# Kernel optimization log

Hardware: AMD Instinct MI355X
Metric: run time of the kernel (lower is better)

The kernel has to match this reference:

```python
import jax, jax.numpy as jnp
import numpy as np

B, C, H, W = 32, 256, 64, 64
K = 7  # kernel_size

def setup_inputs() -> dict:
    key = jax.random.key(0)
    kx, kw = jax.random.split(key)
    x = jax.random.normal(kx, (B, C, H, W), dtype=jnp.float32)
    # Conv2d(2, 1, 7, bias=False) weight: [out_ch=1, in_ch=2, 7, 7]
    w = jax.random.normal(kw, (1, 2, K, K), dtype=jnp.float32) * (1.0 / np.sqrt(2 * K * K))
    return {"x": x, "w": w}

def reference(x, w):
    # channel-wise max and mean, keepdim -> [B,1,H,W]
    max_out = jnp.max(x, axis=1, keepdims=True)
    avg_out = jnp.mean(x, axis=1, keepdims=True)
    concat = jnp.concatenate([max_out, avg_out], axis=1)  # [B,2,H,W]
    pad = K // 2
    conv = jax.lax.conv_general_dilated(
        concat, w,
        window_strides=(1, 1),
        padding=[(pad, pad), (pad, pad)],
        dimension_numbers=("NCHW", "OIHW", "NCHW"),
    )  # [B,1,H,W]
    scale = jax.nn.sigmoid(conv)
    return x * scale  # broadcast over channels
```

## Files before the change

kernel.cpp:

```cpp
#include <hip/hip_runtime.h>
#include <math.h>

constexpr int Bn  = 32;
constexpr int Cn  = 256;
constexpr int Hn  = 64;
constexpr int Wn  = 64;
constexpr int HW  = Hn * Wn;
constexpr int CHW = Cn * HW;
constexpr int HW4 = HW / 4;
constexpr int NPOS  = Bn * HW;
constexpr int NPOS4 = NPOS / 4;

__global__ __launch_bounds__(256) void reduce_k(const float* __restrict__ x,
                                                float* __restrict__ pmax,
                                                float* __restrict__ pavg) {
    __shared__ float4 smax[4][64];
    __shared__ float4 ssum[4][64];

    const int lane  = threadIdx.x & 63;
    const int chunk = threadIdx.x >> 6;
    const int pos4  = blockIdx.x * 64 + lane;
    const int b     = pos4 >> 10;
    const int sp4   = pos4 & (HW4 - 1);

    const float4* xp = (const float4*)x + (size_t)b * (CHW / 4)
                       + (size_t)(chunk * 64) * HW4 + sp4;

    float4 mx = make_float4(-INFINITY, -INFINITY, -INFINITY, -INFINITY);
    float4 sm = make_float4(0.f, 0.f, 0.f, 0.f);

    #pragma unroll 8
    for (int c = 0; c < 64; ++c) {
        float4 v = xp[(size_t)c * HW4];
        mx.x = fmaxf(mx.x, v.x); mx.y = fmaxf(mx.y, v.y);
        mx.z = fmaxf(mx.z, v.z); mx.w = fmaxf(mx.w, v.w);
        sm.x += v.x; sm.y += v.y; sm.z += v.z; sm.w += v.w;
    }

    smax[chunk][lane] = mx;
    ssum[chunk][lane] = sm;
    __syncthreads();

    if (chunk == 0) {
        float4 M = smax[0][lane];
        float4 S = ssum[0][lane];
        #pragma unroll
        for (int k = 1; k < 4; ++k) {
            float4 m2 = smax[k][lane];
            float4 s2 = ssum[k][lane];
            M.x = fmaxf(M.x, m2.x); M.y = fmaxf(M.y, m2.y);
            M.z = fmaxf(M.z, m2.z); M.w = fmaxf(M.w, m2.w);
            S.x += s2.x; S.y += s2.y; S.z += s2.z; S.w += s2.w;
        }
        const float inv = 1.0f / (float)Cn;
        float4 A = make_float4(S.x * inv, S.y * inv, S.z * inv, S.w * inv);
        ((float4*)pmax)[pos4] = M;
        ((float4*)pavg)[pos4] = A;
    }
}

__global__ __launch_bounds__(256) void conv_k(const float* __restrict__ pmax,
                                              const float* __restrict__ pavg,
                                              const float* __restrict__ w,
                                              float* __restrict__ scale) {
    __shared__ float sw[98];
    if (threadIdx.x < 98) sw[threadIdx.x] = w[threadIdx.x];
    __syncthreads();

    const int idx = blockIdx.x * blockDim.x + threadIdx.x;
    const int b   = idx >> 12;
    const int sp  = idx & 4095;
    const int h   = sp >> 6;
    const int wc  = sp & 63;

    const float* pm = pmax + b * HW;
    const float* pa = pavg + b * HW;

    float acc = 0.f;
    #pragma unroll
    for (int kh = 0; kh < 7; ++kh) {
        const int hh = h + kh - 3;
        if (hh < 0 || hh >= Hn) continue;
        #pragma unroll
        for (int kw = 0; kw < 7; ++kw) {
            const int ww = wc + kw - 3;
            if (ww < 0 || ww >= Wn) continue;
            const int o = hh * Wn + ww;
            acc += pm[o] * sw[kh * 7 + kw] + pa[o] * sw[49 + kh * 7 + kw];
        }
    }
    scale[idx] = 1.f / (1.f + expf(-acc));
}

__global__ __launch_bounds__(256) void mul_k(const float* __restrict__ x,
                                             const float* __restrict__ scale,
                                             float* __restrict__ out) {
    const long long i4 = (long long)blockIdx.x * 256 + threadIdx.x;
    const int b   = (int)(i4 >> 18);
    const int hw4 = (int)(i4 & (HW4 - 1));

    const float4 s = ((const float4*)scale)[b * HW4 + hw4];
    const float4 v = ((const float4*)x)[i4];
    float4 o;
    o.x = v.x * s.x; o.y = v.y * s.y; o.z = v.z * s.z; o.w = v.w * s.w;
    ((float4*)out)[i4] = o;
}

extern "C" void kernel_launch(void* const* d_in, const int* in_sizes, int n_in,
                              void* d_out, int out_size, void* d_ws, size_t ws_size,
                              hipStream_t stream) {
    const float* x = (const float*)d_in[0];
    const float* w = (const float*)d_in[1];
    float* out = (float*)d_out;

    float* pmax  = (float*)d_ws;
    float* pavg  = pmax + NPOS;
    float* scale = pavg + NPOS;

    reduce_k<<<NPOS4 / 64, 256, 0, stream>>>(x, pmax, pavg);

    conv_k<<<NPOS / 256, 256, 0, stream>>>(pmax, pavg, w, scale);

    mul_k<<<(Bn * CHW / 4) / 256, 256, 0, stream>>>(x, scale, out);
}
```

Measured before the change: 253.1 us.

## Fuse reduce, conv and multiply into one cooperative kernel with grid syncs

```diff
diff --git a/kernel.cpp b/kernel.cpp
--- a/kernel.cpp
+++ b/kernel.cpp
@@ -1,5 +1,8 @@
 #include <hip/hip_runtime.h>
+#include <hip/hip_cooperative_groups.h>
 #include <math.h>
+
+namespace cg = cooperative_groups;
 
 constexpr int Bn  = 32;
 constexpr int Cn  = 256;
@@ -10,6 +13,119 @@
 constexpr int HW4 = HW / 4;
 constexpr int NPOS  = Bn * HW;
 constexpr int NPOS4 = NPOS / 4;
+
+constexpr int GRID = 512;
+constexpr int BLK  = 256;
+
+__global__ __launch_bounds__(BLK) void fused_k(const float* __restrict__ x,
+                                               const float* __restrict__ w,
+                                               float* __restrict__ out,
+                                               float* __restrict__ pmax,
+                                               float* __restrict__ pavg,
+                                               float* __restrict__ scale) {
+    __shared__ float4 smax[4][64];
+    __shared__ float4 ssum[4][64];
+    __shared__ float  sw[98];
+
+    const int tid = threadIdx.x;
+    if (tid < 98) sw[tid] = w[tid];
+
+    {
+        const int lane  = tid & 63;
+        const int chunk = tid >> 6;
+        const int pos4  = blockIdx.x * 64 + lane;
+        const int b     = pos4 >> 10;
+        const int sp4   = pos4 & (HW4 - 1);
+
+        const float4* xp = (const float4*)x + (size_t)b * (CHW / 4)
+                           + (size_t)(chunk * 64) * HW4 + sp4;
+
+        float4 mx = make_float4(-INFINITY, -INFINITY, -INFINITY, -INFINITY);
+        float4 sm = make_float4(0.f, 0.f, 0.f, 0.f);
+
+        #pragma unroll 8
+        for (int c = 0; c < 64; ++c) {
+            float4 v = xp[(size_t)c * HW4];
+            mx.x = fmaxf(mx.x, v.x); mx.y = fmaxf(mx.y, v.y);
+            mx.z = fmaxf(mx.z, v.z); mx.w = fmaxf(mx.w, v.w);
+            sm.x += v.x; sm.y += v.y; sm.z += v.z; sm.w += v.w;
+        }
+
+        smax[chunk][lane] = mx;
+        ssum[chunk][lane] = sm;
+        __syncthreads();
+
+        if (chunk == 0) {
+            float4 M = smax[0][lane];
+            float4 S = ssum[0][lane];
+            #pragma unroll
+            for (int k = 1; k < 4; ++k) {
+                float4 m2 = smax[k][lane];
+                float4 s2 = ssum[k][lane];
+                M.x = fmaxf(M.x, m2.x); M.y = fmaxf(M.y, m2.y);
+                M.z = fmaxf(M.z, m2.z); M.w = fmaxf(M.w, m2.w);
+                S.x += s2.x; S.y += s2.y; S.z += s2.z; S.w += s2.w;
+            }
+            const float inv = 1.0f / (float)Cn;
+            float4 A = make_float4(S.x * inv, S.y * inv, S.z * inv, S.w * inv);
+            ((float4*)pmax)[pos4] = M;
+            ((float4*)pavg)[pos4] = A;
+        }
+    }
+
+    cg::this_grid().sync();
+
+    {
+        const int idx = blockIdx.x * BLK + tid;
+        const int b   = idx >> 12;
+        const int sp  = idx & 4095;
+        const int h   = sp >> 6;
+        const int wc  = sp & 63;
+
+        const float* pm = pmax + b * HW;
+        const float* pa = pavg + b * HW;
+
+        float acc = 0.f;
+        #pragma unroll
+        for (int kh = 0; kh < 7; ++kh) {
+            const int hh = h + kh - 3;
+            if (hh < 0 || hh >= Hn) continue;
+            #pragma unroll
+            for (int kw = 0; kw < 7; ++kw) {
+                const int ww = wc + kw - 3;
+                if (ww < 0 || ww >= Wn) continue;
+                const int o = hh * Wn + ww;
+                acc += pm[o] * sw[kh * 7 + kw] + pa[o] * sw[49 + kh * 7 + kw];
+            }
+        }
+        scale[idx] = 1.f / (1.f + expf(-acc));
+    }
+
+    cg::this_grid().sync();
+
+    {
+        const int t     = blockIdx.x * BLK + tid;
+        const int hw4   = t & (HW4 - 1);
+        const int cgrp  = t >> 10;
+        const float4* x4 = (const float4*)x;
+        const float4* s4 = (const float4*)scale;
+        float4* o4 = (float4*)out;
+
+        for (int b = 0; b < Bn; ++b) {
+            const float4 s = s4[(b << 10) + hw4];
+            #pragma unroll
+            for (int k = 0; k < 2; ++k) {
+                const size_t i4 = (size_t)b * (CHW / 4)
+                                + (size_t)(cgrp + (k << 7)) * HW4 + hw4;
+                const float4 v = x4[i4];
+                float4 o;
+                o.x = v.x * s.x; o.y = v.y * s.y;
+                o.z = v.z * s.z; o.w = v.w * s.w;
+                o4[i4] = o;
+            }
+        }
+    }
+}
 
 __global__ __launch_bounds__(256) void reduce_k(const float* __restrict__ x,
                                                 float* __restrict__ pmax,
@@ -117,9 +233,15 @@
     float* pavg  = pmax + NPOS;
     float* scale = pavg + NPOS;
 
-    reduce_k<<<NPOS4 / 64, 256, 0, stream>>>(x, pmax, pavg);
-
-    conv_k<<<NPOS / 256, 256, 0, stream>>>(pmax, pavg, w, scale);
-
-    mul_k<<<(Bn * CHW / 4) / 256, 256, 0, stream>>>(x, scale, out);
-}
+    void* args[] = { (void*)&x, (void*)&w, (void*)&out,
+                     (void*)&pmax, (void*)&pavg, (void*)&scale };
+
+    hipError_t err = hipLaunchCooperativeKernel((const void*)fused_k,
+                                                dim3(GRID), dim3(BLK),
+                                                args, 0, stream);
+    if (err != hipSuccess) {
+        reduce_k<<<NPOS4 / 64, 256, 0, stream>>>(x, pmax, pavg);
+        conv_k<<<NPOS / 256, 256, 0, stream>>>(pmax, pavg, w, scale);
+        mul_k<<<(Bn * CHW / 4) / 256, 256, 0, stream>>>(x, scale, out);
+    }
+}
```

New measurement: 385.7 us. +52.4%, slower.

## Fuse conv+sigmoid into the broadcast multiply kernel with shared-memory halo tiles

Applied to the files above, without the earlier changes.

```diff
diff --git a/kernel.cpp b/kernel.cpp
--- a/kernel.cpp
+++ b/kernel.cpp
@@ -10,6 +10,13 @@
 constexpr int HW4 = HW / 4;
 constexpr int NPOS  = Bn * HW;
 constexpr int NPOS4 = NPOS / 4;
+
+constexpr int ROWS   = 16;
+constexpr int NSTR   = Hn / ROWS;
+constexpr int CGRP   = 16;
+constexpr int NCG    = Cn / CGRP;
+constexpr int HALO   = 3;
+constexpr int LROWS  = ROWS + 2 * HALO;
 
 __global__ __launch_bounds__(256) void reduce_k(const float* __restrict__ x,
                                                 float* __restrict__ pmax,
@@ -59,51 +66,74 @@
     }
 }
 
-__global__ __launch_bounds__(256) void conv_k(const float* __restrict__ pmax,
-                                              const float* __restrict__ pavg,
-                                              const float* __restrict__ w,
-                                              float* __restrict__ scale) {
+__global__ __launch_bounds__(256, 8) void convmul_k(const float* __restrict__ x,
+                                                    const float* __restrict__ pmax,
+                                                    const float* __restrict__ pavg,
+                                                    const float* __restrict__ w,
+                                                    float* __restrict__ out) {
+    __shared__ float spm[LROWS * Wn];
+    __shared__ float spa[LROWS * Wn];
+    __shared__ float ssc[ROWS * Wn];
     __shared__ float sw[98];
-    if (threadIdx.x < 98) sw[threadIdx.x] = w[threadIdx.x];
-    __syncthreads();
 
-    const int idx = blockIdx.x * blockDim.x + threadIdx.x;
-    const int b   = idx >> 12;
-    const int sp  = idx & 4095;
-    const int h   = sp >> 6;
-    const int wc  = sp & 63;
+    const int tid = threadIdx.x;
+    const int bid = blockIdx.x;
+    const int cg     = bid & (NCG - 1);
+    const int stripe = (bid >> 4) & (NSTR - 1);
+    const int b      = bid >> 6;
+    const int r0     = stripe * ROWS;
+
+    if (tid < 98) sw[tid] = w[tid];
 
     const float* pm = pmax + b * HW;
     const float* pa = pavg + b * HW;
+    for (int i = tid; i < LROWS * Wn; i += 256) {
+        const int lr  = i >> 6;
+        const int col = i & 63;
+        const int gh  = r0 - HALO + lr;
+        const bool ok = (gh >= 0) && (gh < Hn);
+        spm[i] = ok ? pm[gh * Wn + col] : 0.f;
+        spa[i] = ok ? pa[gh * Wn + col] : 0.f;
+    }
+    __syncthreads();
 
-    float acc = 0.f;
     #pragma unroll
-    for (int kh = 0; kh < 7; ++kh) {
-        const int hh = h + kh - 3;
-        if (hh < 0 || hh >= Hn) continue;
+    for (int p = tid; p < ROWS * Wn; p += 256) {
+        const int hl  = p >> 6;
+        const int col = p & 63;
+        float acc = 0.f;
         #pragma unroll
-        for (int kw = 0; kw < 7; ++kw) {
-            const int ww = wc + kw - 3;
-            if (ww < 0 || ww >= Wn) continue;
-            const int o = hh * Wn + ww;
-            acc += pm[o] * sw[kh * 7 + kw] + pa[o] * sw[49 + kh * 7 + kw];
+        for (int kh = 0; kh < 7; ++kh) {
+            const int lr = hl + kh;
+            #pragma unroll
+            for (int kw = 0; kw < 7; ++kw) {
+                const int ww = col + kw - 3;
+                if (ww < 0 || ww >= Wn) continue;
+                const int o = lr * Wn + ww;
+                acc += spm[o] * sw[kh * 7 + kw] + spa[o] * sw[49 + kh * 7 + kw];
+            }
         }
+        ssc[p] = 1.f / (1.f + expf(-acc));
     }
-    scale[idx] = 1.f / (1.f + expf(-acc));
-}
+    __syncthreads();
 
-__global__ __launch_bounds__(256) void mul_k(const float* __restrict__ x,
-                                             const float* __restrict__ scale,
-                                             float* __restrict__ out) {
-    const long long i4 = (long long)blockIdx.x * 256 + threadIdx.x;
-    const int b   = (int)(i4 >> 18);
-    const int hw4 = (int)(i4 & (HW4 - 1));
+    const float4 s = ((const float4*)ssc)[tid];
 
-    const float4 s = ((const float4*)scale)[b * HW4 + hw4];
-    const float4 v = ((const float4*)x)[i4];
-    float4 o;
-    o.x = v.x * s.x; o.y = v.y * s.y; o.z = v.z * s.z; o.w = v.w * s.w;
-    ((float4*)out)[i4] = o;
+    const size_t base = (size_t)b * (CHW / 4)
+                      + (size_t)(cg * CGRP) * HW4
+                      + (size_t)stripe * (ROWS * Wn / 4) + tid;
+    const float4* x4 = (const float4*)x;
+    float4* o4 = (float4*)out;
+
+    #pragma unroll 4
+    for (int ch = 0; ch < CGRP; ++ch) {
+        const size_t i4 = base + (size_t)ch * HW4;
+        const float4 v = x4[i4];
+        float4 o;
+        o.x = v.x * s.x; o.y = v.y * s.y;
+        o.z = v.z * s.z; o.w = v.w * s.w;
+        o4[i4] = o;
+    }
 }
 
 extern "C" void kernel_launch(void* const* d_in, const int* in_sizes, int n_in,
@@ -113,13 +143,10 @@
     const float* w = (const float*)d_in[1];
     float* out = (float*)d_out;
 
-    float* pmax  = (float*)d_ws;
-    float* pavg  = pmax + NPOS;
-    float* scale = pavg + NPOS;
+    float* pmax = (float*)d_ws;
+    float* pavg = pmax + NPOS;
 
     reduce_k<<<NPOS4 / 64, 256, 0, stream>>>(x, pmax, pavg);
 
-    conv_k<<<NPOS / 256, 256, 0, stream>>>(pmax, pavg, w, scale);
-
-    mul_k<<<(Bn * CHW / 4) / 256, 256, 0, stream>>>(x, scale, out);
+    convmul_k<<<Bn * NSTR * NCG, 256, 0, stream>>>(x, pmax, pavg, w, out);
 }
```

Result: slower. 277.5 us (+9.6%).
